# Optimization experiments

Measured on AMD Instinct MI355X. Metric: run time of the kernel, lower is better.

The kernel has to match this reference:

```python
import jax, jax.numpy as jnp
import numpy as np

B, N, DIM, H, DH, K = 4, 2048, 512, 6, 64, 16
KEEP_PROB = 0.9  # 1 - dropout_rate
LOG2PI = float(np.log(2.0 * np.pi))
LOG_PRIOR = float(np.log(1.0 / K))


def setup_inputs() -> dict:
    key = jax.random.key(0)
    ks = jax.random.split(key, 7)
    inputs_q = jax.random.normal(ks[0], (B, N, DIM), dtype=jnp.float32)
    # decoder-style causal mask, shape [B, 1, q_len, kv_len]
    causal = jnp.tril(jnp.ones((N, N), dtype=jnp.float32))
    mask = jnp.broadcast_to(causal[None, None], (B, 1, N, N))
    # dropout keep mask broadcast across the query dim: [B, H, 1, kv_len]
    keep = jax.random.bernoulli(ks[1], KEEP_PROB, (B, H, 1, N)).astype(jnp.float32)
    w_qkv = jax.random.normal(ks[2], (DIM, 3 * H * DH), dtype=jnp.float32) * 0.02
    w_out = jax.random.normal(ks[3], (H * DH, DIM), dtype=jnp.float32) * 0.02
    mu_lookup = jax.random.normal(ks[4], (K, DIM), dtype=jnp.float32)
    logvar_lookup = jax.random.normal(ks[5], (K, DIM), dtype=jnp.float32) * 0.1
    return {
        "inputs_q": inputs_q,
        "mask": mask,
        "keep": keep,
        "w_qkv": w_qkv,
        "w_out": w_out,
        "mu_lookup": mu_lookup,
        "logvar_lookup": logvar_lookup,
    }


def reference(inputs_q, mask, keep, w_qkv, w_out, mu_lookup, logvar_lookup):
    # --- MultiHeadDotProductAttention (self-attn path) ---
    qkv = (inputs_q @ w_qkv).reshape(B, N, 3, H, DH)  # [B,N,3,H,DH]
    q, k, v = qkv[:, :, 0], qkv[:, :, 1], qkv[:, :, 2]
    # bias: 0 where mask > 0, -1e10 elsewhere (note: no 1/sqrt(d) scaling, as in source)
    bias = jnp.where(mask > 0, 0.0, -1e10)
    attn_weights = jnp.einsum('bqhd,bkhd->bhqk', q, k) + bias  # [B,H,N,N]
    attn_weights = jax.nn.softmax(attn_weights, axis=-1)
    # broadcast dropout: mask shared across the query dim
    attn_weights = attn_weights * keep / KEEP_PROB
    attn_out = jnp.einsum('bhqk,bkhd->bqhd', attn_weights, v)
    attn_out = attn_out.reshape(B, N, H * DH) @ w_out  # [B,N,DIM]

    # --- GMM posterior approx q(y|x) ~= p(y|z) (approx_qy_x, vectorized over k) ---
    z = attn_out.mean(axis=1)  # pooled latent, [B,DIM]
    diff = z[:, None, :] - mu_lookup[None]  # [B,K,DIM]
    llh = -0.5 * jnp.sum(
        diff * diff / jnp.exp(logvar_lookup)[None] + logvar_lookup[None] + LOG2PI,
        axis=-1,
    )  # [B,K]
    logLogit_qy_x = llh + LOG_PRIOR
    qy_x = jax.nn.softmax(logLogit_qy_x, axis=1)  # [B,K]

    # combine mixture mean back in so both branches are live in one output
    return attn_out + (qy_x @ mu_lookup)[:, None, :]
```

## Files before the change

### kernel.cpp

```cpp
#include <hip/hip_runtime.h>
#include <cstdint>
#include <cstddef>

#define NH 6
#define NSEQ 2048
#define DIMD 512
#define BATCH 4
#define HD 384
#define LOG2PI_F 1.8378770664093453f
#define LOG2E_F 1.4426950408889634f
#define M12L2_F (-17.312340490667562f)

typedef __attribute__((ext_vector_type(8))) short short8;
typedef __attribute__((ext_vector_type(8))) unsigned short ushort8;
typedef __attribute__((ext_vector_type(4))) unsigned short ushort4v;
typedef __attribute__((ext_vector_type(4))) float floatx4;

__device__ inline unsigned short f2bf(float f){
  unsigned int u = __float_as_uint(f);
  u += 0x7FFFu + ((u>>16)&1u);
  return (unsigned short)(u>>16);
}

__device__ inline float exp2_raw(float x){
  float r; asm("v_exp_f32 %0, %1" : "=v"(r) : "v"(x)); return r;
}

#define GLD16(gp, lp) __builtin_amdgcn_global_load_lds( \
  (const __attribute__((address_space(1))) void*)(gp), \
  (__attribute__((address_space(3))) void*)(lp), 16, 0, 0)

__device__ inline void wtrans_body(
    const float* __restrict__ src, unsigned short* __restrict__ dst,
    int R, int C, int bx, int by, unsigned short* Ls, int t)
{
  const int r = t>>2, c0 = (t&3)*16;
  const int d0 = by*64, n0 = bx*64;
  #pragma unroll
  for (int j=0;j<16;j+=4){
    floatx4 v = *(const floatx4*)(src + (size_t)(d0+r)*C + n0 + c0 + j);
    #pragma unroll
    for(int jj=0;jj<4;jj++) Ls[r*72 + c0+j+jj] = f2bf(v[jj]);
  }
  __syncthreads();
  #pragma unroll
  for (int j=0;j<16;j+=8){
    ushort8 o;
    #pragma unroll
    for(int jj=0;jj<8;jj++) o[jj] = Ls[(c0+j+jj)*72 + r];
    *(ushort8*)(dst + (size_t)(n0+r)*R + d0 + c0 + j) = o;
  }
}

__global__ __launch_bounds__(256) void prep(
    const float* __restrict__ xq, unsigned short* __restrict__ xbf,
    const float* __restrict__ w_qkv, unsigned short* __restrict__ wqT,
    const float* __restrict__ w_out, unsigned short* __restrict__ woT,
    float* __restrict__ z)
{
  __shared__ __attribute__((aligned(16))) unsigned short Ls[64*72];
  const int bid = blockIdx.x, t = threadIdx.x;
  if (bid < 4096){
    if (bid == 0){
      #pragma unroll
      for(int j=0;j<8;j++) z[t*8+j] = 0.f;
    }
    int i = bid*256 + t;
    floatx4 v = *(const floatx4*)(xq + (size_t)i*4);
    ushort4v r;
    #pragma unroll
    for(int j=0;j<4;j++) r[j] = f2bf(v[j]);
    *(ushort4v*)(xbf + (size_t)i*4) = r;
  } else if (bid < 4240){
    int rb = bid - 4096;
    wtrans_body(w_qkv, wqT, 512, 1152, rb%18, rb/18, Ls, t);
  } else {
    int rb = bid - 4240;
    wtrans_body(w_out, woT, 384, 512, rb%8, rb/8, Ls, t);
  }
}

__global__ __launch_bounds__(256) void gemm_qkv(
    const unsigned short* __restrict__ A,
    const unsigned short* __restrict__ Bt,
    const float* __restrict__ keep,
    unsigned short* __restrict__ Qo, unsigned short* __restrict__ Ko,
    unsigned short* __restrict__ Vt)
{
  __shared__ __attribute__((aligned(16))) unsigned short Cs[128*132];
  unsigned short* As = Cs;
  unsigned short* Bs = Cs + 128*64;
  const int tid = threadIdx.x;
  const int w = tid>>6, lane = tid&63;
  const int wr = w>>1, wc = w&1;
  const int quad = lane>>4, l16 = lane&15;
  const int tM = blockIdx.x*128, tN = blockIdx.y*128;
  const int r8 = lane>>3, c8 = (lane&7)*8;
  floatx4 acc[4][4];
  floatx4 zed = {0.f,0.f,0.f,0.f};
  #pragma unroll
  for (int i=0;i<4;i++)
    #pragma unroll
    for(int j=0;j<4;j++) acc[i][j] = zed;

  for (int k0=0; k0<512; k0+=64){
    #pragma unroll
    for (int i=0;i<4;i++){
      int row = w*32 + i*8;
      GLD16(A  + (size_t)(tM+row+r8)*512 + k0 + c8, As + row*64);
      GLD16(Bt + (size_t)(tN+row+r8)*512 + k0 + c8, Bs + row*64);
    }
    __syncthreads();
    #pragma unroll
    for (int kk=0; kk<64; kk+=32){
      short8 af[4], bf[4];
      #pragma unroll
      for(int mt=0;mt<4;mt++)
        af[mt] = *(const short8*)(As + (wr*64+mt*16+l16)*64 + kk + quad*8);
      #pragma unroll
      for(int nt=0;nt<4;nt++)
        bf[nt] = *(const short8*)(Bs + (wc*64+nt*16+l16)*64 + kk + quad*8);
      #pragma unroll
      for(int mt=0;mt<4;mt++)
        #pragma unroll
        for(int nt=0;nt<4;nt++)
          acc[mt][nt] = __builtin_amdgcn_mfma_f32_16x16x32_bf16(af[mt], bf[nt], acc[mt][nt], 0,0,0);
    }
    __syncthreads();
  }
  #pragma unroll
  for(int mt=0;mt<4;mt++)
    #pragma unroll
    for(int nt=0;nt<4;nt++){
      int gcol = tN + wc*64 + nt*16 + l16;
      float qs = (gcol < 384) ? LOG2E_F : 1.0f;
      #pragma unroll
      for(int r=0;r<4;r++)
        Cs[(wr*64+mt*16+quad*4+r)*132 + wc*64+nt*16+l16] = f2bf(acc[mt][nt][r]*qs);
    }
  __syncthreads();
  if (blockIdx.y < 6){
    const int row = tid>>1, colh = (tid&1)*64;
    const int gcol0 = tN + colh;
    const int t = gcol0/384, rem = gcol0 - t*384, h = rem>>6;
    const int grow = tM + row, b = grow>>11, n = grow & 2047;
    unsigned short* dst = (t==0 ? Qo : Ko) + ((size_t)((b*NH+h)*NSEQ+n))*64;
    #pragma unroll
    for(int j=0;j<8;j++)
      *(ushort8*)(dst + j*8) = *(const ushort8*)(Cs + row*132 + colh + j*8);
  } else {
    const int dcol = tid>>1;
    const int nh   = (tid&1)*64;
    const int gcol = tN + dcol;
    const int rem = gcol - 768, h = rem>>6, dh = rem&63;
    const int b = tM>>11, nb = tM & 2047;
    const float* kp = keep + (size_t)(b*NH+h)*NSEQ + nb + nh;
    unsigned short* dst = Vt + ((size_t)((b*NH+h)*64 + dh))*NSEQ + nb + nh;
    #pragma unroll
    for (int j8=0;j8<8;j8++){
      floatx4 k0 = *(const floatx4*)(kp + j8*8);
      floatx4 k1 = *(const floatx4*)(kp + j8*8 + 4);
      ushort8 o;
      #pragma unroll
      for(int u=0;u<4;u++)
        o[u]   = (k0[u] < 0.5f) ? (unsigned short)0 : Cs[(nh + j8*8 + u)*132 + dcol];
      #pragma unroll
      for(int u=0;u<4;u++)
        o[4+u] = (k1[u] < 0.5f) ? (unsigned short)0 : Cs[(nh + j8*8 + 4 + u)*132 + dcol];
      *(ushort8*)(dst + j8*8) = o;
    }
  }
}

__global__ __launch_bounds__(256, 3) void attn_kernel(
    const unsigned short* __restrict__ Qg, const unsigned short* __restrict__ Kg,
    const unsigned short* __restrict__ VtG,
    unsigned short* __restrict__ atp)
{
  __shared__ __attribute__((aligned(16))) float sm[4*32*34 + 128];
  float* Ocs  = sm;
  float* accs = sm + 4*32*34;
  const int tid = threadIdx.x;
  const int w = tid>>6, lane = tid&63;
  const int quad = lane>>4, l16 = lane&15;
  const int bid = blockIdx.x;
  const int idx = bid>>3;
  const int bh  = (bid&7) + 8*(idx % 3);
  const int c   = 63 - idx/3;
  const int b = bh/NH, h = bh - b*NH;
  const unsigned short* Qb = Qg  + (size_t)bh*NSEQ*64;
  const int q0 = c*32;
  const int nkt = (c>>1) + 1;
  const int q_abs0 = q0 + l16;

  const unsigned short* Kl = Kg  + (size_t)bh*NSEQ*64 + (size_t)l16*64 + quad*8;
  const unsigned short* Vl = VtG + (size_t)bh*64*NSEQ + (size_t)l16*NSEQ + quad*8;

  short8 qf[2][2];
  #pragma unroll
  for(int mt=0;mt<2;mt++)
    #pragma unroll
    for(int kc=0;kc<2;kc++)
      qf[mt][kc] = *(const short8*)(Qb + (size_t)(q0+mt*16+l16)*64 + kc*32 + quad*8);

  floatx4 O[2][4];
  float accl[2] = {0.f, 0.f};
  floatx4 zed = {0.f,0.f,0.f,0.f};
  floatx4 m12v = {M12L2_F, M12L2_F, M12L2_F, M12L2_F};
  #pragma unroll
  for(int mt=0;mt<2;mt++)
    #pragma unroll
    for(int dt=0;dt<4;dt++) O[mt][dt] = zed;

  for (int kt = w; kt < nkt; kt += 4){
    const int kB = kt*64;
    short8 vf[2][4];
    const unsigned short* vp0 = Vl + kB;
    #pragma unroll
    for(int kh=0;kh<2;kh++)
      #pragma unroll
      for(int dt=0;dt<4;dt++)
        vf[kh][dt] = *(const short8*)(vp0 + (size_t)dt*32768 + kh*32);

    floatx4 sacc[2][4];
    #pragma unroll
    for(int mt=0;mt<2;mt++)
      #pragma unroll
      for(int nt=0;nt<4;nt++) sacc[mt][nt] = m12v;
    const unsigned short* kp0 = Kl + (size_t)kt*4096;
    #pragma unroll
    for(int nt=0;nt<4;nt++){
      short8 kf0 = *(const short8*)(kp0 + nt*1024);
      short8 kf1 = *(const short8*)(kp0 + nt*1024 + 32);
      #pragma unroll
      for(int mt=0;mt<2;mt++){
        sacc[mt][nt] = __builtin_amdgcn_mfma_f32_16x16x32_bf16(kf0, qf[mt][0], sacc[mt][nt], 0,0,0);
        sacc[mt][nt] = __builtin_amdgcn_mfma_f32_16x16x32_bf16(kf1, qf[mt][1], sacc[mt][nt], 0,0,0);
      }
    }

    const bool dia = (kt == nkt-1);
    #pragma unroll
    for(int mt=0;mt<2;mt++){
      const int qa = q_abs0 + mt*16;
      unsigned int d0[4], d1[4];
      float rs = 0.f;
      #pragma unroll
      for(int nt=0;nt<4;nt++){
        const int key0 = kB + nt*16 + quad*4;
        float p0 = exp2_raw(sacc[mt][nt][0]);
        float p1 = exp2_raw(sacc[mt][nt][1]);
        float p2 = exp2_raw(sacc[mt][nt][2]);
        float p3 = exp2_raw(sacc[mt][nt][3]);
        if (dia){
          p0 = (key0   <= qa) ? p0 : 0.f;
          p1 = (key0+1 <= qa) ? p1 : 0.f;
          p2 = (key0+2 <= qa) ? p2 : 0.f;
          p3 = (key0+3 <= qa) ? p3 : 0.f;
        }
        rs += (p0+p1) + (p2+p3);
        asm("v_cvt_pk_bf16_f32 %0, %1, %2" : "=v"(d0[nt]) : "v"(p0), "v"(p1));
        asm("v_cvt_pk_bf16_f32 %0, %1, %2" : "=v"(d1[nt]) : "v"(p2), "v"(p3));
      }
      accl[mt] += rs;
      #pragma unroll
      for(int kh=0;kh<2;kh++){
        unsigned int x0 = d0[2*kh],   x1 = d1[2*kh];
        unsigned int y0 = d0[2*kh+1], y1 = d1[2*kh+1];
        asm("v_permlane32_swap_b32 %0, %1" : "+v"(x0), "+v"(y0));
        asm("v_permlane16_swap_b32 %0, %1" : "+v"(x0), "+v"(y0));
        asm("v_permlane32_swap_b32 %0, %1" : "+v"(x1), "+v"(y1));
        asm("v_permlane16_swap_b32 %0, %1" : "+v"(x1), "+v"(y1));
        union { unsigned int u[4]; short8 s; } cvt;
        cvt.u[0] = x0; cvt.u[1] = x1; cvt.u[2] = y0; cvt.u[3] = y1;
        short8 pf = cvt.s;
        #pragma unroll
        for(int dt=0;dt<4;dt++)
          O[mt][dt] = __builtin_amdgcn_mfma_f32_16x16x32_bf16(pf, vf[kh][dt], O[mt][dt], 0,0,0);
      }
    }
  }

  #pragma unroll
  for(int mt=0;mt<2;mt++){
    accl[mt] += __shfl_xor(accl[mt], 16, 64);
    accl[mt] += __shfl_xor(accl[mt], 32, 64);
  }
  if (quad == 0){
    accs[w*32 + l16]      = accl[0];
    accs[w*32 + 16 + l16] = accl[1];
  }

  const int orow = tid>>3, oc4 = (tid&7)*4;
  float sc2 = 0.f;
  #pragma unroll
  for (int h2=0; h2<2; ++h2){
    float* Ow = Ocs + w*(32*34);
    #pragma unroll
    for(int mt=0;mt<2;mt++)
      #pragma unroll
      for(int d2=0;d2<2;d2++){
        const int dt = h2*2 + d2;
        #pragma unroll
        for(int r=0;r<4;r++)
          Ow[(mt*16+quad*4+r)*34 + d2*16 + l16] = O[mt][dt][r];
      }
    __syncthreads();
    if (h2 == 0){
      float as = accs[orow] + accs[32+orow] + accs[64+orow] + accs[96+orow];
      sc2 = (1.0f/0.9f) / as;
    }
    float fv[4];
    #pragma unroll
    for(int j=0;j<4;j++) fv[j] = 0.f;
    #pragma unroll
    for(int s=0;s<4;s++){
      const float* p = Ocs + s*(32*34) + orow*34 + oc4;
      #pragma unroll
      for(int j=0;j<4;j++) fv[j] += p[j];
    }
    ushort4v o4;
    #pragma unroll
    for(int j=0;j<4;j++) o4[j] = f2bf(fv[j]*sc2);
    *(ushort4v*)(atp + ((size_t)(b*NSEQ + q0 + orow))*HD + h*64 + h2*32 + oc4) = o4;
    __syncthreads();
  }
}

__global__ __launch_bounds__(256) void gemm_proj(
    const unsigned short* __restrict__ A,
    const unsigned short* __restrict__ Bt,
    float* __restrict__ out,
    float* __restrict__ z)
{
  __shared__ __attribute__((aligned(16))) unsigned short As[128*64];
  __shared__ __attribute__((aligned(16))) unsigned short Bs[128*64];
  const int tid = threadIdx.x;
  const int w = tid>>6, lane = tid&63;
  const int wr = w>>1, wc = w&1;
  const int quad = lane>>4, l16 = lane&15;
  const int tM = blockIdx.x*128, tN = blockIdx.y*128;
  const int r8 = lane>>3, c8 = (lane&7)*8;
  floatx4 acc[4][4];
  floatx4 zed = {0.f,0.f,0.f,0.f};
  #pragma unroll
  for (int i=0;i<4;i++)
    #pragma unroll
    for(int j=0;j<4;j++) acc[i][j] = zed;

  for (int k0=0; k0<384; k0+=64){
    #pragma unroll
    for (int i=0;i<4;i++){
      int row = w*32 + i*8;
      GLD16(A  + (size_t)(tM+row+r8)*384 + k0 + c8, As + row*64);
      GLD16(Bt + (size_t)(tN+row+r8)*384 + k0 + c8, Bs + row*64);
    }
    __syncthreads();
    #pragma unroll
    for (int kk=0; kk<64; kk+=32){
      short8 af[4], bf[4];
      #pragma unroll
      for(int mt=0;mt<4;mt++)
        af[mt] = *(const short8*)(As + (wr*64+mt*16+l16)*64 + kk + quad*8);
      #pragma unroll
      for(int nt=0;nt<4;nt++)
        bf[nt] = *(const short8*)(Bs + (wc*64+nt*16+l16)*64 + kk + quad*8);
      #pragma unroll
      for(int mt=0;mt<4;mt++)
        #pragma unroll
        for(int nt=0;nt<4;nt++)
          acc[mt][nt] = __builtin_amdgcn_mfma_f32_16x16x32_bf16(af[mt], bf[nt], acc[mt][nt], 0,0,0);
    }
    __syncthreads();
  }
  #pragma unroll
  for(int mt=0;mt<4;mt++){
    int grow = tM + wr*64 + mt*16 + quad*4;
    #pragma unroll
    for(int nt=0;nt<4;nt++){
      int gcol = tN + wc*64 + nt*16 + l16;
      #pragma unroll
      for(int r=0;r<4;r++)
        out[(size_t)(grow+r)*512 + gcol] = acc[mt][nt][r];
    }
  }
  #pragma unroll
  for(int nt=0;nt<4;nt++){
    float s = 0.f;
    #pragma unroll
    for(int mt=0;mt<4;mt++)
      #pragma unroll
      for(int r=0;r<4;r++) s += acc[mt][nt][r];
    s += __shfl_xor(s, 16, 64);
    s += __shfl_xor(s, 32, 64);
    if (quad == 0){
      int gcol = tN + wc*64 + nt*16 + l16;
      atomicAdd(&z[(tM>>11)*DIMD + gcol], s);
    }
  }
}

__global__ __launch_bounds__(256) void gmm_add(
    const float* __restrict__ z, const float* __restrict__ mu,
    const float* __restrict__ lv, float* __restrict__ out)
{
  __shared__ float sh[16];
  __shared__ float qy[16];
  const int tid = threadIdx.x, bid = blockIdx.x;
  const int b = bid>>6;
  {
    const int k = tid>>4, li = tid&15;
    float part = 0.f;
    for(int d=li; d<DIMD; d+=16){
      float zz = z[b*DIMD+d] * (1.0f/2048.0f);
      float m = mu[k*DIMD+d], l = lv[k*DIMD+d];
      float diff = zz - m;
      part += diff*diff*__expf(-l) + l + LOG2PI_F;
    }
    #pragma unroll
    for(int off=8;off>=1;off>>=1) part += __shfl_xor(part, off, 64);
    if (li==0) sh[k] = part;
  }
  __syncthreads();
  if (tid<16){
    float logit = -0.5f*sh[tid];
    float mx = logit;
    #pragma unroll
    for(int off=8;off>=1;off>>=1) mx = fmaxf(mx, __shfl_xor(mx, off, 64));
    float e = __expf(logit-mx);
    float se = e;
    #pragma unroll
    for(int off=8;off>=1;off>>=1) se += __shfl_xor(se, off, 64);
    qy[tid] = e/se;
  }
  __syncthreads();

  const int col4 = (tid&127)*4;
  const int rhalf = tid>>7;
  floatx4 cc = {0.f,0.f,0.f,0.f};
  #pragma unroll
  for(int kk=0;kk<16;kk++){
    const float q = qy[kk];
    const float* mp = mu + kk*DIMD + col4;
    cc[0] += q*mp[0]; cc[1] += q*mp[1]; cc[2] += q*mp[2]; cc[3] += q*mp[3];
  }
  float* ob = out + (size_t)bid*32*DIMD + rhalf*DIMD + col4;
  #pragma unroll
  for(int r=0;r<16;r++){
    float* p = ob + (size_t)r*2*DIMD;
    floatx4 a = *(const floatx4*)p;
    a[0]+=cc[0]; a[1]+=cc[1]; a[2]+=cc[2]; a[3]+=cc[3];
    *(floatx4*)p = a;
  }
}

extern "C" void kernel_launch(void* const* d_in, const int* in_sizes, int n_in,
                              void* d_out, int out_size, void* d_ws, size_t ws_size,
                              hipStream_t stream) {
  const float* inputs_q = (const float*)d_in[0];
  const float* keep  = (const float*)d_in[2];
  const float* w_qkv = (const float*)d_in[3];
  const float* w_out = (const float*)d_in[4];
  const float* mu    = (const float*)d_in[5];
  const float* lv    = (const float*)d_in[6];
  float* out = (float*)d_out;
  char* ws = (char*)d_ws;
  size_t off = 0;
  auto alloc = [&](size_t bytes){ void* p = ws + off; off += (bytes + 255) & ~(size_t)255; return p; };
  unsigned short* Qb  = (unsigned short*)alloc((size_t)24*2048*64*2);
  unsigned short* Kb  = (unsigned short*)alloc((size_t)24*2048*64*2);
  unsigned short* Vt  = (unsigned short*)alloc((size_t)24*64*2048*2);
  unsigned short* xbf = (unsigned short*)alloc((size_t)8192*512*2);
  unsigned short* wqT = (unsigned short*)alloc((size_t)1152*512*2);
  unsigned short* woT = (unsigned short*)alloc((size_t)512*384*2);
  unsigned short* atp = (unsigned short*)alloc((size_t)8192*384*2);
  float* z  = (float*)alloc((size_t)4*512*4);

  prep<<<4288, 256, 0, stream>>>(inputs_q, xbf, w_qkv, wqT, w_out, woT, z);
  gemm_qkv<<<dim3(64,9), 256, 0, stream>>>(xbf, wqT, keep, Qb, Kb, Vt);
  attn_kernel<<<1536, 256, 0, stream>>>(Qb, Kb, Vt, atp);
  gemm_proj<<<dim3(64,4), 256, 0, stream>>>(atp, woT, out, z);
  gmm_add<<<256, 256, 0, stream>>>(z, mu, lv, out);
}
```

Measured before the change: 227.4 us.

## Halve attention query tile to 16 rows and double block count

The attention kernel now gives each block 16 query rows instead of 32, doubling the grid to 3072 blocks. Register state shrinks (one M tile, V fragments loaded inside the PV loop), the launch bound rises to 8 blocks per SM, and the epilogue reduces in a single pass. The aim is better occupancy and load balance across the causal triangle. The cost is that K and V tiles are re-read twice as often per query and each MFMA is amortized over fewer rows.

```diff
diff --git a/kernel.cpp b/kernel.cpp
--- a/kernel.cpp
+++ b/kernel.cpp
@@ -172,159 +172,130 @@
   }
 }
 
-__global__ __launch_bounds__(256, 3) void attn_kernel(
+__global__ __launch_bounds__(256, 8) void attn_kernel(
     const unsigned short* __restrict__ Qg, const unsigned short* __restrict__ Kg,
     const unsigned short* __restrict__ VtG,
     unsigned short* __restrict__ atp)
 {
-  __shared__ __attribute__((aligned(16))) float sm[4*32*34 + 128];
+  __shared__ __attribute__((aligned(16))) float sm[4*16*68 + 64];
   float* Ocs  = sm;
-  float* accs = sm + 4*32*34;
+  float* accs = sm + 4*16*68;
   const int tid = threadIdx.x;
   const int w = tid>>6, lane = tid&63;
   const int quad = lane>>4, l16 = lane&15;
   const int bid = blockIdx.x;
   const int idx = bid>>3;
   const int bh  = (bid&7) + 8*(idx % 3);
-  const int c   = 63 - idx/3;
+  const int c   = 127 - idx/3;
   const int b = bh/NH, h = bh - b*NH;
-  const unsigned short* Qb = Qg  + (size_t)bh*NSEQ*64;
-  const int q0 = c*32;
-  const int nkt = (c>>1) + 1;
-  const int q_abs0 = q0 + l16;
+  const int q0 = c*16;
+  const int nkt = (c>>2) + 1;
+  const int qa = q0 + l16;
 
   const unsigned short* Kl = Kg  + (size_t)bh*NSEQ*64 + (size_t)l16*64 + quad*8;
   const unsigned short* Vl = VtG + (size_t)bh*64*NSEQ + (size_t)l16*NSEQ + quad*8;
 
-  short8 qf[2][2];
-  #pragma unroll
-  for(int mt=0;mt<2;mt++)
-    #pragma unroll
-    for(int kc=0;kc<2;kc++)
-      qf[mt][kc] = *(const short8*)(Qb + (size_t)(q0+mt*16+l16)*64 + kc*32 + quad*8);
-
-  floatx4 O[2][4];
-  float accl[2] = {0.f, 0.f};
+  short8 qf[2];
+  #pragma unroll
+  for(int kc=0;kc<2;kc++)
+    qf[kc] = *(const short8*)(Qg + ((size_t)bh*NSEQ + q0 + l16)*64 + kc*32 + quad*8);
+
+  floatx4 O[4];
+  float accl = 0.f;
   floatx4 zed = {0.f,0.f,0.f,0.f};
-  floatx4 m12v = {M12L2_F, M12L2_F, M12L2_F, M12L2_F};
-  #pragma unroll
-  for(int mt=0;mt<2;mt++)
-    #pragma unroll
-    for(int dt=0;dt<4;dt++) O[mt][dt] = zed;
+  #pragma unroll
+  for(int dt=0;dt<4;dt++) O[dt] = zed;
 
   for (int kt = w; kt < nkt; kt += 4){
     const int kB = kt*64;
-    short8 vf[2][4];
-    const unsigned short* vp0 = Vl + kB;
-    #pragma unroll
-    for(int kh=0;kh<2;kh++)
-      #pragma unroll
-      for(int dt=0;dt<4;dt++)
-        vf[kh][dt] = *(const short8*)(vp0 + (size_t)dt*32768 + kh*32);
-
-    floatx4 sacc[2][4];
-    #pragma unroll
-    for(int mt=0;mt<2;mt++)
-      #pragma unroll
-      for(int nt=0;nt<4;nt++) sacc[mt][nt] = m12v;
+
+    floatx4 sacc[4];
+    #pragma unroll
+    for(int nt=0;nt<4;nt++){
+      sacc[nt][0] = M12L2_F; sacc[nt][1] = M12L2_F;
+      sacc[nt][2] = M12L2_F; sacc[nt][3] = M12L2_F;
+    }
     const unsigned short* kp0 = Kl + (size_t)kt*4096;
     #pragma unroll
     for(int nt=0;nt<4;nt++){
       short8 kf0 = *(const short8*)(kp0 + nt*1024);
       short8 kf1 = *(const short8*)(kp0 + nt*1024 + 32);
-      #pragma unroll
-      for(int mt=0;mt<2;mt++){
-        sacc[mt][nt] = __builtin_amdgcn_mfma_f32_16x16x32_bf16(kf0, qf[mt][0], sacc[mt][nt], 0,0,0);
-        sacc[mt][nt] = __builtin_amdgcn_mfma_f32_16x16x32_bf16(kf1, qf[mt][1], sacc[mt][nt], 0,0,0);
+      sacc[nt] = __builtin_amdgcn_mfma_f32_16x16x32_bf16(kf0, qf[0], sacc[nt], 0,0,0);
+      sacc[nt] = __builtin_amdgcn_mfma_f32_16x16x32_bf16(kf1, qf[1], sacc[nt], 0,0,0);
+    }
+
+    const bool dia = (kt == nkt-1);
+    unsigned int d0[4], d1[4];
+    float rs = 0.f;
+    #pragma unroll
+    for(int nt=0;nt<4;nt++){
+      const int key0 = kB + nt*16 + quad*4;
+      float p0 = exp2_raw(sacc[nt][0]);
+      float p1 = exp2_raw(sacc[nt][1]);
+      float p2 = exp2_raw(sacc[nt][2]);
+      float p3 = exp2_raw(sacc[nt][3]);
+      if (dia){
+        p0 = (key0   <= qa) ? p0 : 0.f;
+        p1 = (key0+1 <= qa) ? p1 : 0.f;
+        p2 = (key0+2 <= qa) ? p2 : 0.f;
+        p3 = (key0+3 <= qa) ? p3 : 0.f;
       }
-    }
-
-    const bool dia = (kt == nkt-1);
-    #pragma unroll
-    for(int mt=0;mt<2;mt++){
-      const int qa = q_abs0 + mt*16;
-      unsigned int d0[4], d1[4];
-      float rs = 0.f;
-      #pragma unroll
-      for(int nt=0;nt<4;nt++){
-        const int key0 = kB + nt*16 + quad*4;
-        float p0 = exp2_raw(sacc[mt][nt][0]);
-        float p1 = exp2_raw(sacc[mt][nt][1]);
-        float p2 = exp2_raw(sacc[mt][nt][2]);
-        float p3 = exp2_raw(sacc[mt][nt][3]);
-        if (dia){
-          p0 = (key0   <= qa) ? p0 : 0.f;
-          p1 = (key0+1 <= qa) ? p1 : 0.f;
-          p2 = (key0+2 <= qa) ? p2 : 0.f;
-          p3 = (key0+3 <= qa) ? p3 : 0.f;
-        }
-        rs += (p0+p1) + (p2+p3);
-        asm("v_cvt_pk_bf16_f32 %0, %1, %2" : "=v"(d0[nt]) : "v"(p0), "v"(p1));
-        asm("v_cvt_pk_bf16_f32 %0, %1, %2" : "=v"(d1[nt]) : "v"(p2), "v"(p3));
+      rs += (p0+p1) + (p2+p3);
+      asm("v_cvt_pk_bf16_f32 %0, %1, %2" : "=v"(d0[nt]) : "v"(p0), "v"(p1));
+      asm("v_cvt_pk_bf16_f32 %0, %1, %2" : "=v"(d1[nt]) : "v"(p2), "v"(p3));
+    }
+    accl += rs;
+
+    #pragma unroll
+    for(int kh=0;kh<2;kh++){
+      unsigned int x0 = d0[2*kh],   x1 = d1[2*kh];
+      unsigned int y0 = d0[2*kh+1], y1 = d1[2*kh+1];
+      asm("v_permlane32_swap_b32 %0, %1" : "+v"(x0), "+v"(y0));
+      asm("v_permlane16_swap_b32 %0, %1" : "+v"(x0), "+v"(y0));
+      asm("v_permlane32_swap_b32 %0, %1" : "+v"(x1), "+v"(y1));
+      asm("v_permlane16_swap_b32 %0, %1" : "+v"(x1), "+v"(y1));
+      union { unsigned int u[4]; short8 s; } cvt;
+      cvt.u[0] = x0; cvt.u[1] = x1; cvt.u[2] = y0; cvt.u[3] = y1;
+      short8 pf = cvt.s;
+      const unsigned short* vp0 = Vl + kB + kh*32;
+      #pragma unroll
+      for(int dt=0;dt<4;dt++){
+        short8 vf = *(const short8*)(vp0 + (size_t)dt*32768);
+        O[dt] = __builtin_amdgcn_mfma_f32_16x16x32_bf16(pf, vf, O[dt], 0,0,0);
       }
-      accl[mt] += rs;
-      #pragma unroll
-      for(int kh=0;kh<2;kh++){
-        unsigned int x0 = d0[2*kh],   x1 = d1[2*kh];
-        unsigned int y0 = d0[2*kh+1], y1 = d1[2*kh+1];
-        asm("v_permlane32_swap_b32 %0, %1" : "+v"(x0), "+v"(y0));
-        asm("v_permlane16_swap_b32 %0, %1" : "+v"(x0), "+v"(y0));
-        asm("v_permlane32_swap_b32 %0, %1" : "+v"(x1), "+v"(y1));
-        asm("v_permlane16_swap_b32 %0, %1" : "+v"(x1), "+v"(y1));
-        union { unsigned int u[4]; short8 s; } cvt;
-        cvt.u[0] = x0; cvt.u[1] = x1; cvt.u[2] = y0; cvt.u[3] = y1;
-        short8 pf = cvt.s;
-        #pragma unroll
-        for(int dt=0;dt<4;dt++)
-          O[mt][dt] = __builtin_amdgcn_mfma_f32_16x16x32_bf16(pf, vf[kh][dt], O[mt][dt], 0,0,0);
-      }
-    }
-  }
-
-  #pragma unroll
-  for(int mt=0;mt<2;mt++){
-    accl[mt] += __shfl_xor(accl[mt], 16, 64);
-    accl[mt] += __shfl_xor(accl[mt], 32, 64);
-  }
-  if (quad == 0){
-    accs[w*32 + l16]      = accl[0];
-    accs[w*32 + 16 + l16] = accl[1];
-  }
-
-  const int orow = tid>>3, oc4 = (tid&7)*4;
-  float sc2 = 0.f;
-  #pragma unroll
-  for (int h2=0; h2<2; ++h2){
-    float* Ow = Ocs + w*(32*34);
-    #pragma unroll
-    for(int mt=0;mt<2;mt++)
-      #pragma unroll
-      for(int d2=0;d2<2;d2++){
-        const int dt = h2*2 + d2;
-        #pragma unroll
-        for(int r=0;r<4;r++)
-          Ow[(mt*16+quad*4+r)*34 + d2*16 + l16] = O[mt][dt][r];
-      }
-    __syncthreads();
-    if (h2 == 0){
-      float as = accs[orow] + accs[32+orow] + accs[64+orow] + accs[96+orow];
-      sc2 = (1.0f/0.9f) / as;
-    }
-    float fv[4];
-    #pragma unroll
-    for(int j=0;j<4;j++) fv[j] = 0.f;
-    #pragma unroll
-    for(int s=0;s<4;s++){
-      const float* p = Ocs + s*(32*34) + orow*34 + oc4;
-      #pragma unroll
-      for(int j=0;j<4;j++) fv[j] += p[j];
-    }
-    ushort4v o4;
-    #pragma unroll
-    for(int j=0;j<4;j++) o4[j] = f2bf(fv[j]*sc2);
-    *(ushort4v*)(atp + ((size_t)(b*NSEQ + q0 + orow))*HD + h*64 + h2*32 + oc4) = o4;
-    __syncthreads();
-  }
+    }
+  }
+
+  accl += __shfl_xor(accl, 16, 64);
+  accl += __shfl_xor(accl, 32, 64);
+  if (quad == 0) accs[w*16 + l16] = accl;
+
+  {
+    float* Ow = Ocs + w*(16*68);
+    #pragma unroll
+    for(int dt=0;dt<4;dt++)
+      #pragma unroll
+      for(int r=0;r<4;r++)
+        Ow[(quad*4+r)*68 + dt*16 + l16] = O[dt][r];
+  }
+  __syncthreads();
+
+  const int orow = tid>>4, oc4 = (tid&15)*4;
+  float as = accs[orow] + accs[16+orow] + accs[32+orow] + accs[48+orow];
+  float sc2 = (1.0f/0.9f) / as;
+  float fv[4];
+  #pragma unroll
+  for(int j=0;j<4;j++) fv[j] = 0.f;
+  #pragma unroll
+  for(int s=0;s<4;s++){
+    const float* p = Ocs + s*(16*68) + orow*68 + oc4;
+    #pragma unroll
+    for(int j=0;j<4;j++) fv[j] += p[j];
+  }
+  ushort4v o4;
+  #pragma unroll
+  for(int j=0;j<4;j++) o4[j] = f2bf(fv[j]*sc2);
+  *(ushort4v*)(atp + ((size_t)(b*NSEQ + q0 + orow))*HD + h*64 + oc4) = o4;
 }
 
 __global__ __launch_bounds__(256) void gemm_proj(
@@ -478,7 +449,7 @@
 
   prep<<<4288, 256, 0, stream>>>(inputs_q, xbf, w_qkv, wqT, w_out, woT, z);
   gemm_qkv<<<dim3(64,9), 256, 0, stream>>>(xbf, wqT, keep, Qb, Kb, Vt);
-  attn_kernel<<<1536, 256, 0, stream>>>(Qb, Kb, Vt, atp);
+  attn_kernel<<<3072, 256, 0, stream>>>(Qb, Kb, Vt, atp);
   gemm_proj<<<dim3(64,4), 256, 0, stream>>>(atp, woT, out, z);
   gmm_add<<<256, 256, 0, stream>>>(z, mu, lv, out);
 }
```

Result: slower. 273.8 us (+20.4%).
